# Kernel tuning notes

Hardware: AMD Instinct MI355X
Metric: run time of the kernel (lower is better)

The kernel has to match this reference:

```python
import jax, jax.numpy as jnp
import numpy as np

N = 50000   # nodes
E = 800000  # edges (avg degree 16)
D = 128     # hidden dim (GNN_hidden_dim), heads=1
SLOPE = 0.2  # LeakyReLU negative slope (PyG default)


def _w(k, shape, fan_in):
    return jax.random.normal(k, shape, dtype=jnp.float32) * (1.0 / np.sqrt(fan_in))


def setup_inputs() -> dict:
    key = jax.random.key(0)
    ks = jax.random.split(key, 24)
    inp = {}
    inp["x"] = jax.random.normal(ks[0], (N, D), dtype=jnp.float32)
    inp["edge_index"] = jax.random.randint(ks[1], (2, E), 0, N, dtype=jnp.int32)
    # layer 1 (GATv2 + linear skip)
    inp["Wl1"] = _w(ks[2], (D, D), D); inp["Wr1"] = _w(ks[3], (D, D), D)
    inp["att1"] = _w(ks[4], (D,), D); inp["b1"] = jnp.zeros((D,), jnp.float32)
    inp["Wlin1"] = _w(ks[5], (D, D), D); inp["blin1"] = jnp.zeros((D,), jnp.float32)
    # layer 2
    inp["Wl2"] = _w(ks[6], (D, D), D); inp["Wr2"] = _w(ks[7], (D, D), D)
    inp["att2"] = _w(ks[8], (D,), D); inp["b2"] = jnp.zeros((D,), jnp.float32)
    inp["Wlin2"] = _w(ks[9], (D, D), D); inp["blin2"] = jnp.zeros((D,), jnp.float32)
    # output layer (out_channels=1, heads=1)
    inp["Wlo"] = _w(ks[10], (D, 1), D); inp["Wro"] = _w(ks[11], (D, 1), D)
    inp["atto"] = _w(ks[12], (1,), 1); inp["bo"] = jnp.zeros((1,), jnp.float32)
    inp["Wlino"] = _w(ks[13], (D, 1), D); inp["blino"] = jnp.zeros((1,), jnp.float32)
    return inp


def gatv2(x, src, dst, Wl, Wr, att, b):
    # GATv2 (PyG, add_self_loops=False, share_weights=False, heads=1, no edge_attr)
    xl = x @ Wl            # [N, C] source transform (also message content)
    xr = x @ Wr            # [N, C] target transform
    e = jax.nn.leaky_relu(xl[src] + xr[dst], SLOPE) @ att  # [E] edge logits
    m = jax.ops.segment_max(e, dst, num_segments=N)
    m = jnp.where(jnp.isfinite(m), m, 0.0)  # empty segments
    p = jnp.exp(e - m[dst])
    s = jax.ops.segment_sum(p, dst, num_segments=N)
    alpha = p / (s[dst] + 1e-16)            # segment softmax over incoming edges
    out = jax.ops.segment_sum(alpha[:, None] * xl[src], dst, num_segments=N)
    return out + b


def reference(x, edge_index, Wl1, Wr1, att1, b1, Wlin1, blin1,
              Wl2, Wr2, att2, b2, Wlin2, blin2,
              Wlo, Wro, atto, bo, Wlino, blino):
    src, dst = edge_index[0], edge_index[1]
    h = jax.nn.relu(gatv2(x, src, dst, Wl1, Wr1, att1, b1) + x @ Wlin1 + blin1)
    h = jax.nn.relu(gatv2(h, src, dst, Wl2, Wr2, att2, b2) + h @ Wlin2 + blin2)
    out = gatv2(h, src, dst, Wlo, Wro, atto, bo) + h @ Wlino + blino
    return out  # [N, 1]
```

## Files before the change

kernel.cpp:

```cpp
#include <hip/hip_runtime.h>
#include <hip/hip_bf16.h>
#include <math.h>

#define NN 50000
#define EE 800000
#define DD 128
#define SLOPE 0.2f

typedef __attribute__((ext_vector_type(8))) short short8;
typedef __attribute__((ext_vector_type(4))) float f32x4;

static __device__ __forceinline__ float wred_sum(float v) {
#pragma unroll
    for (int m = 1; m < 64; m <<= 1) v += __shfl_xor(v, m, 64);
    return v;
}

static __device__ __forceinline__ ushort f2bf(float f) {
    __hip_bfloat16 b = __float2bfloat16(f);
    return *reinterpret_cast<ushort*>(&b);
}
static __device__ __forceinline__ float bf2f(unsigned int u) {
    return __uint_as_float((u & 0xffffu) << 16);
}
static __device__ __forceinline__ void unpack8(const uint4& xp, float* xv) {
    xv[0] = bf2f(xp.x); xv[1] = bf2f(xp.x >> 16);
    xv[2] = bf2f(xp.y); xv[3] = bf2f(xp.y >> 16);
    xv[4] = bf2f(xp.z); xv[5] = bf2f(xp.z >> 16);
    xv[6] = bf2f(xp.w); xv[7] = bf2f(xp.w >> 16);
}

__global__ void k_degree(const int* __restrict__ dstv, int* __restrict__ deg,
                         int* __restrict__ epos) {
    int i = blockIdx.x * blockDim.x + threadIdx.x;
    if (i < EE) epos[i] = atomicAdd(&deg[dstv[i]], 1);
}

__global__ void k_blocksum(const int* __restrict__ deg, int* __restrict__ bsum) {
    int t = threadIdx.x;
    int idx = blockIdx.x * 256 + t;
    int v = (idx < NN) ? deg[idx] : 0;
#pragma unroll
    for (int m = 1; m < 64; m <<= 1) v += __shfl_xor(v, m, 64);
    __shared__ int part[4];
    if ((t & 63) == 0) part[t >> 6] = v;
    __syncthreads();
    if (t == 0) bsum[blockIdx.x] = part[0] + part[1] + part[2] + part[3];
}

__global__ void k_scan_bsum(const int* __restrict__ bsum, int* __restrict__ boff, int nb) {
    __shared__ int sd[2][256];
    int t = threadIdx.x;
    int v = (t < nb) ? bsum[t] : 0;
    sd[0][t] = v;
    __syncthreads();
    int s = 0;
    for (int off = 1; off < 256; off <<= 1) {
        int x = sd[s][t];
        if (t >= off) x += sd[s][t - off];
        sd[s ^ 1][t] = x;
        s ^= 1;
        __syncthreads();
    }
    if (t < nb) boff[t] = sd[s][t] - v;
}

__global__ void k_scan_final(const int* __restrict__ deg, const int* __restrict__ boff,
                             int* __restrict__ offs) {
    __shared__ int sd[2][256];
    int t = threadIdx.x;
    int idx = blockIdx.x * 256 + t;
    int v = (idx < NN) ? deg[idx] : 0;
    sd[0][t] = v;
    __syncthreads();
    int s = 0;
    for (int off = 1; off < 256; off <<= 1) {
        int x = sd[s][t];
        if (t >= off) x += sd[s][t - off];
        sd[s ^ 1][t] = x;
        s ^= 1;
        __syncthreads();
    }
    int incl = sd[s][t];
    int base = boff[blockIdx.x];
    if (idx < NN) offs[idx + 1] = base + incl;
    if (idx == 0) offs[0] = 0;
}

__global__ void k_scatter(const int* __restrict__ srcv, const int* __restrict__ dstv,
                          const int* __restrict__ offs, const int* __restrict__ epos,
                          int* __restrict__ csr_src) {
    int i = blockIdx.x * blockDim.x + threadIdx.x;
    if (i < EE) csr_src[offs[dstv[i]] + epos[i]] = srcv[i];
}

__global__ __launch_bounds__(256) void k_wconvert(
    const float* __restrict__ W0, const float* __restrict__ W1, const float* __restrict__ W2,
    const float* __restrict__ W3, const float* __restrict__ W4, const float* __restrict__ W5,
    ushort* __restrict__ Wt) {
    int idx = blockIdx.x * 256 + threadIdx.x;
    int i = idx >> 14;
    int r = idx & 16383;
    int n = r >> 7;
    int k = r & 127;
    const float* Ws[6] = {W0, W1, W2, W3, W4, W5};
    Wt[idx] = f2bf(Ws[i][k * DD + n]);
}

template <int XBF>
__global__ __launch_bounds__(256) void k_gemm3m(
    const float* __restrict__ Xf,
    const ushort* __restrict__ Xb,
    const ushort* __restrict__ Wt,
    ushort* __restrict__ O0b,
    ushort* __restrict__ O1b,
    ushort* __restrict__ O2b) {
    __shared__ ushort wsh[128 * 136];
    int t = threadIdx.x;
    int wid = t >> 6, lane = t & 63;
    int m0 = blockIdx.x * 128 + wid * 32;
    int qrow = lane & 15, kg = lane >> 4;

    short8 afrag[2][4];
#pragma unroll
    for (int mg = 0; mg < 2; mg++) {
#pragma unroll
        for (int ks = 0; ks < 4; ks++) {
            int row = m0 + mg * 16 + qrow;
            row = (row < NN) ? row : (NN - 1);
            if (XBF) {
                afrag[mg][ks] = *reinterpret_cast<const short8*>(
                    Xb + (size_t)row * DD + ks * 32 + kg * 8);
            } else {
                const float* p = Xf + (size_t)row * DD + ks * 32 + kg * 8;
                float4 u0 = *reinterpret_cast<const float4*>(p);
                float4 u1 = *reinterpret_cast<const float4*>(p + 4);
                short8 s;
                s[0] = (short)f2bf(u0.x); s[1] = (short)f2bf(u0.y);
                s[2] = (short)f2bf(u0.z); s[3] = (short)f2bf(u0.w);
                s[4] = (short)f2bf(u1.x); s[5] = (short)f2bf(u1.y);
                s[6] = (short)f2bf(u1.z); s[7] = (short)f2bf(u1.w);
                afrag[mg][ks] = s;
            }
        }
    }

    for (int w = 0; w < 3; w++) {
        __syncthreads();
        const ushort* Wb = Wt + (size_t)w * DD * DD;
#pragma unroll
        for (int i = 0; i < 8; i++) {
            int flat = i * 256 + t;
            int row = flat >> 4, ch = flat & 15;
            short8 v = *reinterpret_cast<const short8*>(Wb + row * DD + ch * 8);
            *reinterpret_cast<short8*>(&wsh[row * 136 + ch * 8]) = v;
        }
        __syncthreads();

        f32x4 acc[2][8];
#pragma unroll
        for (int mg = 0; mg < 2; mg++)
#pragma unroll
            for (int ng = 0; ng < 8; ng++) acc[mg][ng] = (f32x4)(0.f);

#pragma unroll
        for (int ks = 0; ks < 4; ks++) {
            short8 bfrag[8];
#pragma unroll
            for (int ng = 0; ng < 8; ng++)
                bfrag[ng] = *reinterpret_cast<const short8*>(
                    &wsh[(ng * 16 + qrow) * 136 + ks * 32 + kg * 8]);
#pragma unroll
            for (int mg = 0; mg < 2; mg++)
#pragma unroll
                for (int ng = 0; ng < 8; ng++)
                    acc[mg][ng] = __builtin_amdgcn_mfma_f32_16x16x32_bf16(
                        afrag[mg][ks], bfrag[ng], acc[mg][ng], 0, 0, 0);
        }

        ushort* Ob = (w == 0) ? O0b : (w == 1) ? O1b : O2b;
#pragma unroll
        for (int mg = 0; mg < 2; mg++) {
#pragma unroll
            for (int r = 0; r < 4; r++) {
                int row = m0 + mg * 16 + kg * 4 + r;
                if (row < NN) {
#pragma unroll
                    for (int ng = 0; ng < 8; ng++) {
                        int col = ng * 16 + qrow;
                        Ob[(size_t)row * DD + col] = f2bf(acc[mg][ng][r]);
                    }
                }
            }
        }
    }
}

template <int OUTVEC>
__global__ __launch_bounds__(64) void k_fused(
    const int* __restrict__ offs, const int* __restrict__ csr_src,
    const ushort* __restrict__ xlb,
    const ushort* __restrict__ xrb,
    const float* __restrict__ att,
    const ushort* __restrict__ linb,
    const float* __restrict__ bb,
    const float* __restrict__ blin, ushort* __restrict__ houtb,
    const float* __restrict__ Wlo, const float* __restrict__ Wro,
    const float* __restrict__ Wlino, const float* __restrict__ blino,
    float* __restrict__ xlo, float* __restrict__ xro, float* __restrict__ lino) {
    int wid = blockIdx.x;
    int lane = threadIdx.x;
    int q = lane >> 4;
    int ql = lane & 15;
    int c0 = ql * 8;

    float av6[8], av4[8];
    {
        float4 a0 = *reinterpret_cast<const float4*>(att + c0);
        float4 a1 = *reinterpret_cast<const float4*>(att + c0 + 4);
        float av[8] = {a0.x, a0.y, a0.z, a0.w, a1.x, a1.y, a1.z, a1.w};
#pragma unroll
        for (int c = 0; c < 8; c++) {
            av6[c] = 0.6f * av[c];
            av4[c] = 0.4f * av[c];
        }
    }
    float xrv[8];
    {
        uint4 xrp = *reinterpret_cast<const uint4*>(xrb + (size_t)wid * DD + c0);
        unpack8(xrp, xrv);
    }

    int start = offs[wid];
    int deg = offs[wid + 1] - start;

    float ss = 0.f;
    float acc[8];
#pragma unroll
    for (int c = 0; c < 8; c++) acc[c] = 0.f;

    for (int eb = 0; eb < deg; eb += 64) {
        int nb = min(64, deg - eb);
        int myidx = (lane < nb) ? csr_src[start + eb + lane] : 0;
        int rounds = (nb + 3) >> 2;
        for (int r = 0; r < rounds; r++) {
            int j = r * 4 + q;
            bool ok = j < nb;
            int s = __shfl(myidx, j, 64);
            uint4 xp = *reinterpret_cast<const uint4*>(xlb + (size_t)s * DD + c0);
            float xv[8];
            unpack8(xp, xv);
            float v = 0.f;
#pragma unroll
            for (int c = 0; c < 8; c++) {
                float u = xv[c] + xrv[c];
                v = __builtin_fmaf(u, av6[c], v);
                v = __builtin_fmaf(__builtin_fabsf(u), av4[c], v);
            }
#pragma unroll
            for (int msk = 1; msk < 16; msk <<= 1) v += __shfl_xor(v, msk, 64);
            float p = ok ? __expf(v) : 0.f;
            ss += p;
#pragma unroll
            for (int c = 0; c < 8; c++) acc[c] += p * xv[c];
        }
    }

#pragma unroll
    for (int msk = 16; msk < 64; msk <<= 1) {
        ss += __shfl_xor(ss, msk, 64);
#pragma unroll
        for (int c = 0; c < 8; c++) acc[c] += __shfl_xor(acc[c], msk, 64);
    }

    if (q == 0) {
        float inv = 1.f / (ss + 1e-16f);
        float lv[8];
        {
            uint4 lp = *reinterpret_cast<const uint4*>(linb + (size_t)wid * DD + c0);
            unpack8(lp, lv);
        }
        float4 b0 = *reinterpret_cast<const float4*>(bb + c0);
        float4 b1 = *reinterpret_cast<const float4*>(bb + c0 + 4);
        float4 bl0 = *reinterpret_cast<const float4*>(blin + c0);
        float4 bl1 = *reinterpret_cast<const float4*>(blin + c0 + 4);
        float bv[8] = {b0.x, b0.y, b0.z, b0.w, b1.x, b1.y, b1.z, b1.w};
        float blv[8] = {bl0.x, bl0.y, bl0.z, bl0.w, bl1.x, bl1.y, bl1.z, bl1.w};
        float o[8];
#pragma unroll
        for (int c = 0; c < 8; c++) o[c] = fmaxf(acc[c] * inv + bv[c] + lv[c] + blv[c], 0.f);

        if (!OUTVEC) {
            uint4 pk;
            pk.x = (unsigned)f2bf(o[0]) | ((unsigned)f2bf(o[1]) << 16);
            pk.y = (unsigned)f2bf(o[2]) | ((unsigned)f2bf(o[3]) << 16);
            pk.z = (unsigned)f2bf(o[4]) | ((unsigned)f2bf(o[5]) << 16);
            pk.w = (unsigned)f2bf(o[6]) | ((unsigned)f2bf(o[7]) << 16);
            *reinterpret_cast<uint4*>(houtb + (size_t)wid * DD + c0) = pk;
        } else {
            float4 w0a = *reinterpret_cast<const float4*>(Wlo + c0);
            float4 w0b = *reinterpret_cast<const float4*>(Wlo + c0 + 4);
            float4 w1a = *reinterpret_cast<const float4*>(Wro + c0);
            float4 w1b = *reinterpret_cast<const float4*>(Wro + c0 + 4);
            float4 w2a = *reinterpret_cast<const float4*>(Wlino + c0);
            float4 w2b = *reinterpret_cast<const float4*>(Wlino + c0 + 4);
            float wv0[8] = {w0a.x, w0a.y, w0a.z, w0a.w, w0b.x, w0b.y, w0b.z, w0b.w};
            float wv1[8] = {w1a.x, w1a.y, w1a.z, w1a.w, w1b.x, w1b.y, w1b.z, w1b.w};
            float wv2[8] = {w2a.x, w2a.y, w2a.z, w2a.w, w2b.x, w2b.y, w2b.z, w2b.w};
            float d0 = 0.f, d1 = 0.f, d2 = 0.f;
#pragma unroll
            for (int c = 0; c < 8; c++) {
                d0 += o[c] * wv0[c];
                d1 += o[c] * wv1[c];
                d2 += o[c] * wv2[c];
            }
#pragma unroll
            for (int msk = 1; msk < 16; msk <<= 1) {
                d0 += __shfl_xor(d0, msk, 64);
                d1 += __shfl_xor(d1, msk, 64);
                d2 += __shfl_xor(d2, msk, 64);
            }
            if (ql == 0) {
                xlo[wid] = d0;
                xro[wid] = d1;
                lino[wid] = d2 + blino[0];
            }
        }
    }
}

__global__ __launch_bounds__(256) void k_aggout(
    const int* __restrict__ offs, const int* __restrict__ csr_src,
    const float* __restrict__ xlo, const float* __restrict__ xro,
    const float* __restrict__ atto, const float* __restrict__ lino,
    const float* __restrict__ bo, float* __restrict__ out) {
    int wid = (blockIdx.x * blockDim.x + threadIdx.x) >> 6;
    int lane = threadIdx.x & 63;
    if (wid >= NN) return;
    int start = offs[wid];
    int deg = offs[wid + 1] - start;
    float xro_w = xro[wid];
    float a0 = atto[0];

    float sl = 0.f, nl = 0.f;
    for (int j = lane; j < deg; j += 64) {
        int s = csr_src[start + j];
        float xs = xlo[s];
        float u = xs + xro_w;
        float e = fmaxf(u, SLOPE * u) * a0;
        float p = __expf(e);
        sl += p;
        nl += p * xs;
    }
    sl = wred_sum(sl);
    nl = wred_sum(nl);
    if (lane == 0) out[wid] = nl / (sl + 1e-16f) + bo[0] + lino[wid];
}

extern "C" void kernel_launch(void* const* d_in, const int* in_sizes, int n_in,
                              void* d_out, int out_size, void* d_ws, size_t ws_size,
                              hipStream_t stream) {
    const float* x = (const float*)d_in[0];
    const int* ei = (const int*)d_in[1];
    const int* srcv = ei;
    const int* dstv = ei + EE;
    const float* Wl1 = (const float*)d_in[2];
    const float* Wr1 = (const float*)d_in[3];
    const float* att1 = (const float*)d_in[4];
    const float* b1 = (const float*)d_in[5];
    const float* Wlin1 = (const float*)d_in[6];
    const float* blin1 = (const float*)d_in[7];
    const float* Wl2 = (const float*)d_in[8];
    const float* Wr2 = (const float*)d_in[9];
    const float* att2 = (const float*)d_in[10];
    const float* b2 = (const float*)d_in[11];
    const float* Wlin2 = (const float*)d_in[12];
    const float* blin2 = (const float*)d_in[13];
    const float* Wlo = (const float*)d_in[14];
    const float* Wro = (const float*)d_in[15];
    const float* atto = (const float*)d_in[16];
    const float* bo = (const float*)d_in[17];
    const float* Wlino = (const float*)d_in[18];
    const float* blino = (const float*)d_in[19];

    char* w = (char*)d_ws;
    auto alloc = [&](size_t bytes) {
        void* p = (void*)w;
        w += (bytes + 255) & ~(size_t)255;
        return p;
    };
    ushort* xlb = (ushort*)alloc((size_t)NN * DD * 2);
    ushort* xrb = (ushort*)alloc((size_t)NN * DD * 2);
    ushort* linb = (ushort*)alloc((size_t)NN * DD * 2);
    ushort* hb = (ushort*)alloc((size_t)NN * DD * 2);
    ushort* Wt = (ushort*)alloc((size_t)6 * DD * DD * 2);
    float* xlo = (float*)alloc((size_t)NN * 4);
    float* xro = (float*)alloc((size_t)NN * 4);
    float* lino = (float*)alloc((size_t)NN * 4);
    int* deg = (int*)alloc((size_t)NN * 4);
    int* offs = (int*)alloc((size_t)(NN + 1) * 4);
    int* bsum = (int*)alloc(256 * 4);
    int* boff = (int*)alloc(256 * 4);
    int* csr_src = (int*)alloc((size_t)(EE + 64) * 4);
    int* epos = (int*)alloc((size_t)EE * 4);

    const int NB = (NN + 255) / 256;

    hipMemsetAsync(deg, 0, (size_t)NN * 4, stream);
    k_degree<<<(EE + 255) / 256, 256, 0, stream>>>(dstv, deg, epos);
    k_blocksum<<<NB, 256, 0, stream>>>(deg, bsum);
    k_scan_bsum<<<1, 256, 0, stream>>>(bsum, boff, NB);
    k_scan_final<<<NB, 256, 0, stream>>>(deg, boff, offs);
    k_scatter<<<(EE + 255) / 256, 256, 0, stream>>>(srcv, dstv, offs, epos, csr_src);

    k_wconvert<<<(6 * DD * DD) / 256, 256, 0, stream>>>(Wl1, Wr1, Wlin1, Wl2, Wr2, Wlin2, Wt);

    const int GEMM_GRID = (NN + 127) / 128;
    const int NODE_GRID = (NN * 64 + 255) / 256;

    k_gemm3m<0><<<GEMM_GRID, 256, 0, stream>>>(x, nullptr, Wt + (size_t)0 * 3 * DD * DD,
                                               xlb, xrb, linb);
    k_fused<0><<<NN, 64, 0, stream>>>(offs, csr_src, xlb, xrb, att1, linb, b1, blin1, hb,
                                      nullptr, nullptr, nullptr, nullptr,
                                      nullptr, nullptr, nullptr);
    k_gemm3m<1><<<GEMM_GRID, 256, 0, stream>>>(nullptr, hb, Wt + (size_t)1 * 3 * DD * DD,
                                               xlb, xrb, linb);
    k_fused<1><<<NN, 64, 0, stream>>>(offs, csr_src, xlb, xrb, att2, linb, b2, blin2,
                                      nullptr, Wlo, Wro, Wlino, blino,
                                      xlo, xro, lino);
    k_aggout<<<NODE_GRID, 256, 0, stream>>>(offs, csr_src, xlo, xro, atto, lino, bo, (float*)d_out);
}
```

Before: 192.1 us.

## Switch intermediates to fp16 with packed half2 edge math; single-block scan

Converts stored activations and weights from bf16 to fp16, uses fp16 MFMA, and performs the per-edge logit and weighted-accumulation math with packed half2 FMAs instead of unpacked fp32. This is meant to halve ALU work in the gather-heavy fused kernel. Separately, the three-kernel degree prefix scan is replaced with a single 1024-thread block scan, cutting launch count. The fp16 accumulation of softmax-weighted sums risks precision loss and overflow, since the exp weights are not max-shifted.

```diff
diff --git a/kernel.cpp b/kernel.cpp
--- a/kernel.cpp
+++ b/kernel.cpp
@@ -1,5 +1,5 @@
 #include <hip/hip_runtime.h>
-#include <hip/hip_bf16.h>
+#include <hip/hip_fp16.h>
 #include <math.h>
 
 #define NN 50000
@@ -7,7 +7,7 @@
 #define DD 128
 #define SLOPE 0.2f
 
-typedef __attribute__((ext_vector_type(8))) short short8;
+typedef __attribute__((ext_vector_type(8))) _Float16 half8;
 typedef __attribute__((ext_vector_type(4))) float f32x4;
 
 static __device__ __forceinline__ float wred_sum(float v) {
@@ -16,18 +16,21 @@
     return v;
 }
 
-static __device__ __forceinline__ ushort f2bf(float f) {
-    __hip_bfloat16 b = __float2bfloat16(f);
-    return *reinterpret_cast<ushort*>(&b);
-}
-static __device__ __forceinline__ float bf2f(unsigned int u) {
-    return __uint_as_float((u & 0xffffu) << 16);
-}
-static __device__ __forceinline__ void unpack8(const uint4& xp, float* xv) {
-    xv[0] = bf2f(xp.x); xv[1] = bf2f(xp.x >> 16);
-    xv[2] = bf2f(xp.y); xv[3] = bf2f(xp.y >> 16);
-    xv[4] = bf2f(xp.z); xv[5] = bf2f(xp.z >> 16);
-    xv[6] = bf2f(xp.w); xv[7] = bf2f(xp.w >> 16);
+static __device__ __forceinline__ ushort f2h(float f) {
+    __half h = __float2half(f);
+    return *reinterpret_cast<ushort*>(&h);
+}
+static __device__ __forceinline__ float h2f(ushort u) {
+    __half h = *reinterpret_cast<__half*>(&u);
+    return __half2float(h);
+}
+static __device__ __forceinline__ __half2 u2h2(unsigned int u) {
+    __half2 h;
+    *reinterpret_cast<unsigned int*>(&h) = u;
+    return h;
+}
+static __device__ __forceinline__ unsigned int h22u(__half2 h) {
+    return *reinterpret_cast<unsigned int*>(&h);
 }
 
 __global__ void k_degree(const int* __restrict__ dstv, int* __restrict__ deg,
@@ -36,55 +39,37 @@
     if (i < EE) epos[i] = atomicAdd(&deg[dstv[i]], 1);
 }
 
-__global__ void k_blocksum(const int* __restrict__ deg, int* __restrict__ bsum) {
+#define SCAN_T 1024
+#define SCAN_CH ((NN + SCAN_T - 1) / SCAN_T)
+__global__ __launch_bounds__(1024) void k_scan(const int* __restrict__ deg,
+                                               int* __restrict__ offs) {
+    __shared__ int sd[2][SCAN_T];
     int t = threadIdx.x;
-    int idx = blockIdx.x * 256 + t;
-    int v = (idx < NN) ? deg[idx] : 0;
-#pragma unroll
-    for (int m = 1; m < 64; m <<= 1) v += __shfl_xor(v, m, 64);
-    __shared__ int part[4];
-    if ((t & 63) == 0) part[t >> 6] = v;
-    __syncthreads();
-    if (t == 0) bsum[blockIdx.x] = part[0] + part[1] + part[2] + part[3];
-}
-
-__global__ void k_scan_bsum(const int* __restrict__ bsum, int* __restrict__ boff, int nb) {
-    __shared__ int sd[2][256];
-    int t = threadIdx.x;
-    int v = (t < nb) ? bsum[t] : 0;
-    sd[0][t] = v;
+    int base = t * SCAN_CH;
+    int sum = 0;
+    for (int i = 0; i < SCAN_CH; i++) {
+        int idx = base + i;
+        if (idx < NN) sum += deg[idx];
+    }
+    sd[0][t] = sum;
     __syncthreads();
     int s = 0;
-    for (int off = 1; off < 256; off <<= 1) {
+    for (int off = 1; off < SCAN_T; off <<= 1) {
         int x = sd[s][t];
         if (t >= off) x += sd[s][t - off];
         sd[s ^ 1][t] = x;
         s ^= 1;
         __syncthreads();
     }
-    if (t < nb) boff[t] = sd[s][t] - v;
-}
-
-__global__ void k_scan_final(const int* __restrict__ deg, const int* __restrict__ boff,
-                             int* __restrict__ offs) {
-    __shared__ int sd[2][256];
-    int t = threadIdx.x;
-    int idx = blockIdx.x * 256 + t;
-    int v = (idx < NN) ? deg[idx] : 0;
-    sd[0][t] = v;
-    __syncthreads();
-    int s = 0;
-    for (int off = 1; off < 256; off <<= 1) {
-        int x = sd[s][t];
-        if (t >= off) x += sd[s][t - off];
-        sd[s ^ 1][t] = x;
-        s ^= 1;
-        __syncthreads();
-    }
-    int incl = sd[s][t];
-    int base = boff[blockIdx.x];
-    if (idx < NN) offs[idx + 1] = base + incl;
-    if (idx == 0) offs[0] = 0;
+    int run = sd[s][t] - sum;
+    for (int i = 0; i < SCAN_CH; i++) {
+        int idx = base + i;
+        if (idx < NN) {
+            offs[idx] = run;
+            run += deg[idx];
+        }
+    }
+    if (base < NN && base + SCAN_CH >= NN) offs[NN] = run;
 }
 
 __global__ void k_scatter(const int* __restrict__ srcv, const int* __restrict__ dstv,
@@ -104,7 +89,7 @@
     int n = r >> 7;
     int k = r & 127;
     const float* Ws[6] = {W0, W1, W2, W3, W4, W5};
-    Wt[idx] = f2bf(Ws[i][k * DD + n]);
+    Wt[idx] = f2h(Ws[i][k * DD + n]);
 }
 
 template <int XBF>
@@ -121,7 +106,7 @@
     int m0 = blockIdx.x * 128 + wid * 32;
     int qrow = lane & 15, kg = lane >> 4;
 
-    short8 afrag[2][4];
+    half8 afrag[2][4];
 #pragma unroll
     for (int mg = 0; mg < 2; mg++) {
 #pragma unroll
@@ -129,17 +114,17 @@
             int row = m0 + mg * 16 + qrow;
             row = (row < NN) ? row : (NN - 1);
             if (XBF) {
-                afrag[mg][ks] = *reinterpret_cast<const short8*>(
+                afrag[mg][ks] = *reinterpret_cast<const half8*>(
                     Xb + (size_t)row * DD + ks * 32 + kg * 8);
             } else {
                 const float* p = Xf + (size_t)row * DD + ks * 32 + kg * 8;
                 float4 u0 = *reinterpret_cast<const float4*>(p);
                 float4 u1 = *reinterpret_cast<const float4*>(p + 4);
-                short8 s;
-                s[0] = (short)f2bf(u0.x); s[1] = (short)f2bf(u0.y);
-                s[2] = (short)f2bf(u0.z); s[3] = (short)f2bf(u0.w);
-                s[4] = (short)f2bf(u1.x); s[5] = (short)f2bf(u1.y);
-                s[6] = (short)f2bf(u1.z); s[7] = (short)f2bf(u1.w);
+                half8 s;
+                s[0] = (_Float16)u0.x; s[1] = (_Float16)u0.y;
+                s[2] = (_Float16)u0.z; s[3] = (_Float16)u0.w;
+                s[4] = (_Float16)u1.x; s[5] = (_Float16)u1.y;
+                s[6] = (_Float16)u1.z; s[7] = (_Float16)u1.w;
                 afrag[mg][ks] = s;
             }
         }
@@ -152,8 +137,8 @@
         for (int i = 0; i < 8; i++) {
             int flat = i * 256 + t;
             int row = flat >> 4, ch = flat & 15;
-            short8 v = *reinterpret_cast<const short8*>(Wb + row * DD + ch * 8);
-            *reinterpret_cast<short8*>(&wsh[row * 136 + ch * 8]) = v;
+            half8 v = *reinterpret_cast<const half8*>(Wb + row * DD + ch * 8);
+            *reinterpret_cast<half8*>(&wsh[row * 136 + ch * 8]) = v;
         }
         __syncthreads();
 
@@ -165,16 +150,16 @@
 
 #pragma unroll
         for (int ks = 0; ks < 4; ks++) {
-            short8 bfrag[8];
+            half8 bfrag[8];
 #pragma unroll
             for (int ng = 0; ng < 8; ng++)
-                bfrag[ng] = *reinterpret_cast<const short8*>(
+                bfrag[ng] = *reinterpret_cast<const half8*>(
                     &wsh[(ng * 16 + qrow) * 136 + ks * 32 + kg * 8]);
 #pragma unroll
             for (int mg = 0; mg < 2; mg++)
 #pragma unroll
                 for (int ng = 0; ng < 8; ng++)
-                    acc[mg][ng] = __builtin_amdgcn_mfma_f32_16x16x32_bf16(
+                    acc[mg][ng] = __builtin_amdgcn_mfma_f32_16x16x32_f16(
                         afrag[mg][ks], bfrag[ng], acc[mg][ng], 0, 0, 0);
         }
 
@@ -188,7 +173,7 @@
 #pragma unroll
                     for (int ng = 0; ng < 8; ng++) {
                         int col = ng * 16 + qrow;
-                        Ob[(size_t)row * DD + col] = f2bf(acc[mg][ng][r]);
+                        Ob[(size_t)row * DD + col] = f2h(acc[mg][ng][r]);
                     }
                 }
             }
@@ -214,30 +199,33 @@
     int ql = lane & 15;
     int c0 = ql * 8;
 
-    float av6[8], av4[8];
+    __half2 av6h[4], av4h[4];
     {
         float4 a0 = *reinterpret_cast<const float4*>(att + c0);
         float4 a1 = *reinterpret_cast<const float4*>(att + c0 + 4);
         float av[8] = {a0.x, a0.y, a0.z, a0.w, a1.x, a1.y, a1.z, a1.w};
 #pragma unroll
-        for (int c = 0; c < 8; c++) {
-            av6[c] = 0.6f * av[c];
-            av4[c] = 0.4f * av[c];
-        }
-    }
-    float xrv[8];
+        for (int c = 0; c < 4; c++) {
+            av6h[c] = __halves2half2(__float2half(0.6f * av[2 * c]),
+                                     __float2half(0.6f * av[2 * c + 1]));
+            av4h[c] = __halves2half2(__float2half(0.4f * av[2 * c]),
+                                     __float2half(0.4f * av[2 * c + 1]));
+        }
+    }
+    __half2 xrv2[4];
     {
         uint4 xrp = *reinterpret_cast<const uint4*>(xrb + (size_t)wid * DD + c0);
-        unpack8(xrp, xrv);
+        xrv2[0] = u2h2(xrp.x); xrv2[1] = u2h2(xrp.y);
+        xrv2[2] = u2h2(xrp.z); xrv2[3] = u2h2(xrp.w);
     }
 
     int start = offs[wid];
     int deg = offs[wid + 1] - start;
 
     float ss = 0.f;
-    float acc[8];
-#pragma unroll
-    for (int c = 0; c < 8; c++) acc[c] = 0.f;
+    __half2 acc2[4];
+#pragma unroll
+    for (int c = 0; c < 4; c++) acc2[c] = u2h2(0u);
 
     for (int eb = 0; eb < deg; eb += 64) {
         int nb = min(64, deg - eb);
@@ -248,21 +236,23 @@
             bool ok = j < nb;
             int s = __shfl(myidx, j, 64);
             uint4 xp = *reinterpret_cast<const uint4*>(xlb + (size_t)s * DD + c0);
-            float xv[8];
-            unpack8(xp, xv);
-            float v = 0.f;
-#pragma unroll
-            for (int c = 0; c < 8; c++) {
-                float u = xv[c] + xrv[c];
-                v = __builtin_fmaf(u, av6[c], v);
-                v = __builtin_fmaf(__builtin_fabsf(u), av4[c], v);
-            }
+            __half2 xv2[4] = {u2h2(xp.x), u2h2(xp.y), u2h2(xp.z), u2h2(xp.w)};
+            __half2 vs = u2h2(0u);
+#pragma unroll
+            for (int c = 0; c < 4; c++) {
+                __half2 u2 = __hadd2(xv2[c], xrv2[c]);
+                __half2 a2 = u2h2(h22u(u2) & 0x7fff7fffu);
+                vs = __hfma2(u2, av6h[c], vs);
+                vs = __hfma2(a2, av4h[c], vs);
+            }
+            float v = __low2float(vs) + __high2float(vs);
 #pragma unroll
             for (int msk = 1; msk < 16; msk <<= 1) v += __shfl_xor(v, msk, 64);
             float p = ok ? __expf(v) : 0.f;
             ss += p;
-#pragma unroll
-            for (int c = 0; c < 8; c++) acc[c] += p * xv[c];
+            __half2 p2 = __float2half2_rn(p);
+#pragma unroll
+            for (int c = 0; c < 4; c++) acc2[c] = __hfma2(p2, xv2[c], acc2[c]);
         }
     }
 
@@ -270,15 +260,29 @@
     for (int msk = 16; msk < 64; msk <<= 1) {
         ss += __shfl_xor(ss, msk, 64);
 #pragma unroll
-        for (int c = 0; c < 8; c++) acc[c] += __shfl_xor(acc[c], msk, 64);
+        for (int c = 0; c < 4; c++) {
+            unsigned int o = (unsigned int)__shfl_xor((int)h22u(acc2[c]), msk, 64);
+            acc2[c] = __hadd2(acc2[c], u2h2(o));
+        }
     }
 
     if (q == 0) {
         float inv = 1.f / (ss + 1e-16f);
+        float o[8];
+#pragma unroll
+        for (int c = 0; c < 4; c++) {
+            o[2 * c] = __low2float(acc2[c]) * inv;
+            o[2 * c + 1] = __high2float(acc2[c]) * inv;
+        }
         float lv[8];
         {
             uint4 lp = *reinterpret_cast<const uint4*>(linb + (size_t)wid * DD + c0);
-            unpack8(lp, lv);
+            __half2 l2[4] = {u2h2(lp.x), u2h2(lp.y), u2h2(lp.z), u2h2(lp.w)};
+#pragma unroll
+            for (int c = 0; c < 4; c++) {
+                lv[2 * c] = __low2float(l2[c]);
+                lv[2 * c + 1] = __high2float(l2[c]);
+            }
         }
         float4 b0 = *reinterpret_cast<const float4*>(bb + c0);
         float4 b1 = *reinterpret_cast<const float4*>(bb + c0 + 4);
@@ -286,16 +290,15 @@
         float4 bl1 = *reinterpret_cast<const float4*>(blin + c0 + 4);
         float bv[8] = {b0.x, b0.y, b0.z, b0.w, b1.x, b1.y, b1.z, b1.w};
         float blv[8] = {bl0.x, bl0.y, bl0.z, bl0.w, bl1.x, bl1.y, bl1.z, bl1.w};
-        float o[8];
-#pragma unroll
-        for (int c = 0; c < 8; c++) o[c] = fmaxf(acc[c] * inv + bv[c] + lv[c] + blv[c], 0.f);
+#pragma unroll
+        for (int c = 0; c < 8; c++) o[c] = fmaxf(o[c] + bv[c] + lv[c] + blv[c], 0.f);
 
         if (!OUTVEC) {
             uint4 pk;
-            pk.x = (unsigned)f2bf(o[0]) | ((unsigned)f2bf(o[1]) << 16);
-            pk.y = (unsigned)f2bf(o[2]) | ((unsigned)f2bf(o[3]) << 16);
-            pk.z = (unsigned)f2bf(o[4]) | ((unsigned)f2bf(o[5]) << 16);
-            pk.w = (unsigned)f2bf(o[6]) | ((unsigned)f2bf(o[7]) << 16);
+            pk.x = (unsigned)f2h(o[0]) | ((unsigned)f2h(o[1]) << 16);
+            pk.y = (unsigned)f2h(o[2]) | ((unsigned)f2h(o[3]) << 16);
+            pk.z = (unsigned)f2h(o[4]) | ((unsigned)f2h(o[5]) << 16);
+            pk.w = (unsigned)f2h(o[6]) | ((unsigned)f2h(o[7]) << 16);
             *reinterpret_cast<uint4*>(houtb + (size_t)wid * DD + c0) = pk;
         } else {
             float4 w0a = *reinterpret_cast<const float4*>(Wlo + c0);
@@ -399,18 +402,12 @@
     float* lino = (float*)alloc((size_t)NN * 4);
     int* deg = (int*)alloc((size_t)NN * 4);
     int* offs = (int*)alloc((size_t)(NN + 1) * 4);
-    int* bsum = (int*)alloc(256 * 4);
-    int* boff = (int*)alloc(256 * 4);
     int* csr_src = (int*)alloc((size_t)(EE + 64) * 4);
     int* epos = (int*)alloc((size_t)EE * 4);
 
-    const int NB = (NN + 255) / 256;
-
     hipMemsetAsync(deg, 0, (size_t)NN * 4, stream);
     k_degree<<<(EE + 255) / 256, 256, 0, stream>>>(dstv, deg, epos);
-    k_blocksum<<<NB, 256, 0, stream>>>(deg, bsum);
-    k_scan_bsum<<<1, 256, 0, stream>>>(bsum, boff, NB);
-    k_scan_final<<<NB, 256, 0, stream>>>(deg, boff, offs);
+    k_scan<<<1, 1024, 0, stream>>>(deg, offs);
     k_scatter<<<(EE + 255) / 256, 256, 0, stream>>>(srcv, dstv, offs, epos, csr_src);
 
     k_wconvert<<<(6 * DD * DD) / 256, 256, 0, stream>>>(Wl1, Wr1, Wlin1, Wl2, Wr2, Wlin2, Wt);
```

New measurement: 276.4 us. 1.44x slower.
